# Kernel optimization log

Hardware: AMD Instinct MI355X
Metric: run time of the kernel (lower is better)

## Reference

```python
import jax, jax.numpy as jnp
import numpy as np

D_MODEL = 1024
NUM_HEADS = 16
HEAD_DIM = D_MODEL // NUM_HEADS  # 64
ROPE_THETA = 10000.0
BATCH = 2
SEQ = 2048
NEG_INF = -1e30


def setup_inputs() -> dict:
    key = jax.random.key(0)
    ks = jax.random.split(key, 6)
    std = 1.0 / np.sqrt(D_MODEL)
    x = jax.random.normal(ks[0], (BATCH, SEQ, D_MODEL), dtype=jnp.float32)
    wq = jax.random.normal(ks[1], (D_MODEL, D_MODEL), dtype=jnp.float32) * std
    wk = jax.random.normal(ks[2], (D_MODEL, D_MODEL), dtype=jnp.float32) * std
    wv = jax.random.normal(ks[3], (D_MODEL, D_MODEL), dtype=jnp.float32) * std
    wo = jax.random.normal(ks[4], (D_MODEL, D_MODEL), dtype=jnp.float32) * std
    token_positions = jnp.broadcast_to(jnp.arange(SEQ, dtype=jnp.int32)[None, :], (BATCH, SEQ))
    return {"x": x, "token_positions": token_positions, "wq": wq, "wk": wk, "wv": wv, "wo": wo}


def _apply_rope(t, token_positions):
    # t: (B, H, S, head_dim), token_positions: (B, S)
    half = HEAD_DIM // 2
    inv_freq = 1.0 / (ROPE_THETA ** (2.0 * jnp.arange(half, dtype=jnp.float32) / HEAD_DIM))
    angles = token_positions.astype(jnp.float32)[..., None] * inv_freq  # (B, S, half)
    cos = jnp.cos(angles)[:, None, :, :]  # (B, 1, S, half)
    sin = jnp.sin(angles)[:, None, :, :]
    tp = t.reshape(*t.shape[:-1], half, 2)  # interleaved pairs
    x1, x2 = tp[..., 0], tp[..., 1]
    r1 = x1 * cos - x2 * sin
    r2 = x1 * sin + x2 * cos
    return jnp.stack([r1, r2], axis=-1).reshape(t.shape)


def reference(x, token_positions, wq, wk, wv, wo):
    B, S, D = x.shape
    H, hd = NUM_HEADS, HEAD_DIM
    # projections (Linear: y = x @ W.T, no bias)
    q = (x @ wq.T).reshape(B, S, H, hd).transpose(0, 2, 1, 3)  # (B, H, S, hd)
    k = (x @ wk.T).reshape(B, S, H, hd).transpose(0, 2, 1, 3)
    v = (x @ wv.T).reshape(B, S, H, hd).transpose(0, 2, 1, 3)
    # RoPE on Q, K
    q = _apply_rope(q, token_positions)
    k = _apply_rope(k, token_positions)
    # causal scaled dot-product attention
    scores = jnp.einsum("bhqd,bhkd->bhqk", q, k) / jnp.sqrt(jnp.float32(hd))
    mask = jnp.tril(jnp.ones((S, S), dtype=bool))
    scores = jnp.where(mask, scores, NEG_INF)
    probs = jax.nn.softmax(scores, axis=-1)
    attn = jnp.einsum("bhqk,bhkd->bhqd", probs, v)  # (B, H, S, hd)
    attn = attn.transpose(0, 2, 1, 3).reshape(B, S, D)
    return attn @ wo.T
```

## Files before the change

### kernel.cpp

```cpp
#include <hip/hip_runtime.h>
#include <stdint.h>
#include <math.h>

#define SEQ 2048
#define NH 16
#define DM 1024

typedef __bf16 bf16x8 __attribute__((ext_vector_type(8)));
typedef __bf16 bf16x2 __attribute__((ext_vector_type(2)));
typedef short s16x4 __attribute__((ext_vector_type(4)));
typedef short s16x8 __attribute__((ext_vector_type(8)));
typedef float f32x4 __attribute__((ext_vector_type(4)));
typedef float f32x2 __attribute__((ext_vector_type(2)));

#define ASM_VMCNT0  asm volatile("s_waitcnt vmcnt(0)" ::: "memory")
#define ASM_BARRIER asm volatile("s_barrier" ::: "memory")

__device__ __forceinline__ unsigned short f2bf(float f) {
  union { float f; unsigned u; } v; v.f = f;
  unsigned r = v.u + 0x7fffu + ((v.u >> 16) & 1u);
  return (unsigned short)(r >> 16);
}
__device__ __forceinline__ unsigned pk2(float a, float b) {
  f32x2 v = {a, b};
  bf16x2 r = __builtin_convertvector(v, bf16x2);
  union { bf16x2 h; unsigned u; } c; c.h = r;
  return c.u;
}
__device__ __forceinline__ void load_lds16(const void* g, void* l) {
  __builtin_amdgcn_global_load_lds((__attribute__((address_space(1))) void*)g,
                                   (__attribute__((address_space(3))) void*)l,
                                   16, 0, 0);
}

__global__ void cvt_all(const float* __restrict__ x, const float* __restrict__ wq,
                        const float* __restrict__ wk, const float* __restrict__ wv,
                        const float* __restrict__ wo, unsigned short* __restrict__ ws) {
  const int i = blockIdx.x * blockDim.x + threadIdx.x;
  const int off = i * 4;
  const float* src;
  unsigned short* dst;
  if (off < 4194304) {
    src = x + off;  dst = ws + off;
  } else {
    const int r = off - 4194304;
    const int w = r >> 20, o = r & 1048575;
    const float* tabs[4] = {wq, wk, wv, wo};
    src = tabs[w] + o;  dst = ws + 4194304 + (w << 20) + o;
  }
  const float4 v = *(const float4*)src;
  uint2 u;
  u.x = pk2(v.x, v.y);
  u.y = pk2(v.z, v.w);
  *(uint2*)dst = u;
}

__launch_bounds__(256, 3)
__global__ void gemm_qkv(const unsigned short* __restrict__ X,
                         const unsigned short* __restrict__ W3,
                         unsigned short* __restrict__ Qr,
                         unsigned short* __restrict__ Kr,
                         unsigned short* __restrict__ Vt,
                         const int* __restrict__ tp) {
  __shared__ __align__(16) char smem[32768];

  const int t = threadIdx.x;
  const int lane = t & 63, wave = t >> 6;
  const int quad = lane >> 4, l16 = lane & 15;
  const int m0 = blockIdx.y * 128, n0 = blockIdx.x * 128;
  const int wm = (wave >> 1) * 64, wn = (wave & 1) * 64;

  f32x4 acc[4][4];
#pragma unroll
  for (int i = 0; i < 4; i++)
#pragma unroll
    for (int j = 0; j < 4; j++) { acc[i][j][0]=0.f; acc[i][j][1]=0.f; acc[i][j][2]=0.f; acc[i][j][3]=0.f; }

  const int rr = t >> 2;
  const int cc = (t & 3) * 8;

#define QKV_STAGE(bufidx, k0_) do {                                               \
    char* a_ = smem + (bufidx) * 8192;                                            \
    char* b_ = smem + 16384 + (bufidx) * 8192;                                    \
    _Pragma("unroll")                                                             \
    for (int i_ = 0; i_ < 2; i_++) {                                              \
      load_lds16(X  + (uint64_t)(m0 + i_ * 64 + rr) * 1024 + (k0_) + cc,          \
                 a_ + i_ * 4096 + wave * 1024);                                   \
      load_lds16(W3 + (uint64_t)(n0 + i_ * 64 + rr) * 1024 + (k0_) + cc,          \
                 b_ + i_ * 4096 + wave * 1024);                                   \
    }                                                                             \
  } while (0)

  QKV_STAGE(0, 0);

  for (int k0 = 0; k0 < 1024; k0 += 32) {
    const int buf = (k0 >> 5) & 1;
    ASM_VMCNT0;
    ASM_BARRIER;
    if (k0 + 32 < 1024) QKV_STAGE(buf ^ 1, k0 + 32);
    char* As = smem + buf * 8192;
    char* Bs = smem + 16384 + buf * 8192;

    bf16x8 af[4], bfr[4];
#pragma unroll
    for (int i = 0; i < 4; i++) {
      af[i]  = *(const bf16x8*)(As + (wm + i * 16 + l16) * 64 + quad * 16);
      bfr[i] = *(const bf16x8*)(Bs + (wn + i * 16 + l16) * 64 + quad * 16);
    }
#pragma unroll
    for (int i = 0; i < 4; i++)
#pragma unroll
      for (int j = 0; j < 4; j++)
        acc[i][j] = __builtin_amdgcn_mfma_f32_16x16x32_bf16(af[i], bfr[j], acc[i][j], 0, 0, 0);
  }
#undef QKV_STAGE

  if (n0 < 2048) {
    unsigned short* dst = (n0 < 1024) ? Qr : Kr;
    float fr[4]; int dd[4], hh[4];
#pragma unroll
    for (int j = 0; j < 4; j++) {
      const int n = n0 + wn + j * 16 + l16;
      dd[j] = n & 63;
      hh[j] = (n & 1023) >> 6;
      fr[j] = __builtin_amdgcn_exp2f(-0.20762050594f * (float)(dd[j] & ~1)) * 0.15915494309f;
    }
    const float sgnodd = (l16 & 1) ? 1.f : -1.f;
#pragma unroll
    for (int i = 0; i < 4; i++) {
#pragma unroll
      for (int r = 0; r < 4; r++) {
        const int m = m0 + wm + i * 16 + quad * 4 + r;
        const int s = m & 2047, b = m >> 11;
        const float posf = (float)tp[m];
#pragma unroll
        for (int j = 0; j < 4; j++) {
          const float v = acc[i][j][r];
          const float p = __shfl_xor(v, 1);
          float rev = posf * fr[j];
          rev -= floorf(rev);
          float sn, cs;
          asm("v_sin_f32 %0, %1" : "=v"(sn) : "v"(rev));
          asm("v_cos_f32 %0, %1" : "=v"(cs) : "v"(rev));
          const float rv = fmaf(v, cs, p * sn * sgnodd);
          dst[((uint64_t)((b * NH + hh[j]) * SEQ + s)) * 64 + dd[j]] = f2bf(rv);
        }
      }
    }
  } else {
#pragma unroll
    for (int i = 0; i < 4; i++) {
      const int m = m0 + wm + i * 16 + quad * 4;
      const int s = m & 2047, b = m >> 11;
      const int sl = s & 63;
      const int qv = (sl >> 2) & 3, nv = sl >> 4;
      const int g = (s & ~63) + qv * 16 + (nv >> 1) * 8 + (nv & 1) * 4;
#pragma unroll
      for (int j = 0; j < 4; j++) {
        const int n = n0 - 2048 + wn + j * 16 + l16;
        const int h = n >> 6, d = n & 63;
        uint2 w;
        w.x = pk2(acc[i][j][0], acc[i][j][1]);
        w.y = pk2(acc[i][j][2], acc[i][j][3]);
        *(uint2*)(Vt + ((uint64_t)((b * NH + h) * 64 + d)) * SEQ + g) = w;
      }
    }
  }
}

__launch_bounds__(256, 2)
__global__ void gemm_ao(const unsigned short* __restrict__ A,
                        const unsigned short* __restrict__ B,
                        float* __restrict__ C) {
  __shared__ __align__(16) char smem[32768];

  const int t = threadIdx.x;
  const int lane = t & 63, wave = t >> 6;
  const int quad = lane >> 4, l16 = lane & 15;
  const int m0 = blockIdx.y * 128, n0 = blockIdx.x * 128;
  const int wm = (wave >> 1) * 64, wn = (wave & 1) * 64;

  f32x4 acc[4][4];
#pragma unroll
  for (int i = 0; i < 4; i++)
#pragma unroll
    for (int j = 0; j < 4; j++) { acc[i][j][0]=0.f; acc[i][j][1]=0.f; acc[i][j][2]=0.f; acc[i][j][3]=0.f; }

  const int rr = t >> 2;
  const int cc = (t & 3) * 8;

#define AO_STAGE(bufidx, k0_) do {                                               \
    char* a_ = smem + (bufidx) * 8192;                                            \
    char* b_ = smem + 16384 + (bufidx) * 8192;                                    \
    _Pragma("unroll")                                                             \
    for (int i_ = 0; i_ < 2; i_++) {                                              \
      load_lds16(A + (uint64_t)(m0 + i_ * 64 + rr) * 1024 + (k0_) + cc,           \
                 a_ + i_ * 4096 + wave * 1024);                                   \
      load_lds16(B + (uint64_t)(n0 + i_ * 64 + rr) * 1024 + (k0_) + cc,           \
                 b_ + i_ * 4096 + wave * 1024);                                   \
    }                                                                             \
  } while (0)

  AO_STAGE(0, 0);

  for (int k0 = 0; k0 < 1024; k0 += 32) {
    const int buf = (k0 >> 5) & 1;
    ASM_VMCNT0;
    ASM_BARRIER;
    if (k0 + 32 < 1024) AO_STAGE(buf ^ 1, k0 + 32);
    char* As = smem + buf * 8192;
    char* Bs = smem + 16384 + buf * 8192;

    bf16x8 af[4], bfr[4];
#pragma unroll
    for (int i = 0; i < 4; i++) {
      af[i]  = *(const bf16x8*)(As + (wm + i * 16 + l16) * 64 + quad * 16);
      bfr[i] = *(const bf16x8*)(Bs + (wn + i * 16 + l16) * 64 + quad * 16);
    }
#pragma unroll
    for (int i = 0; i < 4; i++)
#pragma unroll
      for (int j = 0; j < 4; j++)
        acc[i][j] = __builtin_amdgcn_mfma_f32_16x16x32_bf16(af[i], bfr[j], acc[i][j], 0, 0, 0);
  }
#undef AO_STAGE

#pragma unroll
  for (int i = 0; i < 4; i++)
#pragma unroll
    for (int j = 0; j < 4; j++)
#pragma unroll
      for (int r = 0; r < 4; r++) {
        const int m = m0 + wm + i * 16 + quad * 4 + r;
        const int n = n0 + wn + j * 16 + l16;
        C[(uint64_t)m * DM + n] = acc[i][j][r];
      }
}

__launch_bounds__(256, 4)
__global__ void flash_attn(const unsigned short* __restrict__ Q,
                           const unsigned short* __restrict__ K,
                           const unsigned short* __restrict__ Vt,
                           unsigned short* __restrict__ Oa) {
  __shared__ __align__(16) char smem[32768];

  const int t = threadIdx.x;
  const int lane = t & 63, wid = t >> 6;
  const int quad = lane >> 4, l16 = lane & 15;
  const int u = blockIdx.x;
  const int tq = 31 - (u >> 5);
  const int bh = u & 31;
  const uint64_t base = (uint64_t)bh * (SEQ * 64);
  const int qb = tq * 64;
  const int ng = tq + 1;
  const int qg = qb + wid * 16 + l16;
  const int b = bh >> 4, h = bh & 15;

  bf16x8 qf[2];
  {
    const unsigned short* qp = Q + base + (uint64_t)qg * 64 + quad * 8;
    qf[0] = *(const bf16x8*)qp;  qf[1] = *(const bf16x8*)(qp + 32);
  }

  f32x4 o[4];
#pragma unroll
  for (int i = 0; i < 4; i++) { o[i][0]=0.f; o[i][1]=0.f; o[i][2]=0.f; o[i][3]=0.f; }
  float lI = 0.f;

  const int sr8 = lane >> 3;
  const int sc = ((lane & 7) ^ sr8) * 8;
  const int swz = (l16 & 7);

#define STAGE(bufidx, kb_) do {                                                   \
    _Pragma("unroll")                                                             \
    for (int i_ = 0; i_ < 2; i_++) {                                              \
      const int r_ = wid * 16 + i_ * 8 + sr8;                                     \
      load_lds16(K  + base + (uint64_t)((kb_) + r_) * 64 + sc,                    \
                 smem + (bufidx) * 8192 + wid * 2048 + i_ * 1024);                \
      load_lds16(Vt + base + (uint64_t)r_ * SEQ + (kb_) + sc,                     \
                 smem + 16384 + (bufidx) * 8192 + wid * 2048 + i_ * 1024);        \
    }                                                                             \
  } while (0)

  STAGE(0, 0);

  const float c1 = 0.18033688011f;

  for (int it = 0; it < ng; it++) {
    const int kb = it * 64;
    const int buf = it & 1;
    ASM_VMCNT0;
    ASM_BARRIER;
    if (it + 1 < ng) STAGE(buf ^ 1, (it + 1) * 64);
    char* ks = smem + buf * 8192;
    char* vs = smem + 16384 + buf * 8192;

    int nbmax = ((qb + wid * 16 + 15 - kb) >> 4) + 1;
    nbmax = nbmax > 4 ? 4 : (nbmax < 0 ? 0 : nbmax);
    const bool diag = (kb + 63) > (qb + wid * 16);

    f32x4 sf[4];
    float ls = 0.f;
#pragma unroll
    for (int nb = 0; nb < 4; nb++) {
      if (nb < nbmax) {
        f32x4 s; s[0]=0.f; s[1]=0.f; s[2]=0.f; s[3]=0.f;
#pragma unroll
        for (int kk = 0; kk < 2; kk++) {
          bf16x8 kfr = *(const bf16x8*)(ks + (nb * 16 + l16) * 128 + (((kk * 4 + quad) ^ swz) * 16));
          s = __builtin_amdgcn_mfma_f32_16x16x32_bf16(kfr, qf[kk], s, 0, 0, 0);
        }
        if (diag) {
#pragma unroll
          for (int r = 0; r < 4; r++) {
            const int key = kb + nb * 16 + quad * 4 + r;
            const float p = (key <= qg) ? __builtin_amdgcn_exp2f(s[r] * c1) : 0.f;
            sf[nb][r] = p;  ls += p;
          }
        } else {
#pragma unroll
          for (int r = 0; r < 4; r++) {
            const float p = __builtin_amdgcn_exp2f(s[r] * c1);
            sf[nb][r] = p;  ls += p;
          }
        }
      }
    }
    lI += ls;

#pragma unroll
    for (int np = 0; np < 2; np++) {
      if (2 * np < nbmax) {
        union { uint2 u; s16x4 h; } p0;
        p0.u.x = pk2(sf[2 * np][0], sf[2 * np][1]);
        p0.u.y = pk2(sf[2 * np][2], sf[2 * np][3]);
        const bool hi = (2 * np + 1 < nbmax);
        union { uint2 u; s16x4 h; } p1;
        if (hi) {
          p1.u.x = pk2(sf[2 * np + 1][0], sf[2 * np + 1][1]);
          p1.u.y = pk2(sf[2 * np + 1][2], sf[2 * np + 1][3]);
        }
#pragma unroll
        for (int db = 0; db < 4; db++) {
          s16x8 vv = *(const s16x8*)(vs + (db * 16 + l16) * 128 +
                                     (((quad * 2 + np) ^ swz) * 16));
          s16x4 vlo = __builtin_shufflevector(vv, vv, 0, 1, 2, 3);
          o[db] = __builtin_amdgcn_mfma_f32_16x16x16bf16_1k(vlo, p0.h, o[db], 0, 0, 0);
          if (hi) {
            s16x4 vhi = __builtin_shufflevector(vv, vv, 4, 5, 6, 7);
            o[db] = __builtin_amdgcn_mfma_f32_16x16x16bf16_1k(vhi, p1.h, o[db], 0, 0, 0);
          }
        }
      }
    }
  }
#undef STAGE

  float lr = lI;
  lr += __shfl_xor(lr, 16);
  lr += __shfl_xor(lr, 32);
  const float invl = 1.0f / lr;
  unsigned short* orow = Oa + ((uint64_t)(b * SEQ + qg)) * DM + h * 64 + quad * 4;
#pragma unroll
  for (int db = 0; db < 4; db++) {
    uint2 w;
    w.x = pk2(o[db][0] * invl, o[db][1] * invl);
    w.y = pk2(o[db][2] * invl, o[db][3] * invl);
    *(uint2*)(orow + db * 16) = w;
  }
}

extern "C" void kernel_launch(void* const* d_in, const int* in_sizes, int n_in,
                              void* d_out, int out_size, void* d_ws, size_t ws_size,
                              hipStream_t stream) {
  const float* x  = (const float*)d_in[0];
  const int* tp   = (const int*)d_in[1];
  const float* wq = (const float*)d_in[2];
  const float* wk = (const float*)d_in[3];
  const float* wv = (const float*)d_in[4];
  const float* wo = (const float*)d_in[5];
  float* out = (float*)d_out;

  unsigned short* ws = (unsigned short*)d_ws;
  unsigned short* xb  = ws;
  unsigned short* w3b = ws + 4194304;
  unsigned short* wob = ws + 7340032;
  unsigned short* Qr  = ws + 8388608;
  unsigned short* Kr  = ws + 12582912;
  unsigned short* Vt  = ws + 16777216;
  unsigned short* At  = ws + 20971520;

  cvt_all<<<8192, 256, 0, stream>>>(x, wq, wk, wv, wo, ws);
  gemm_qkv<<<dim3(24, 32), 256, 0, stream>>>(xb, w3b, Qr, Kr, Vt, tp);
  flash_attn<<<1024, 256, 0, stream>>>(Qr, Kr, Vt, At);
  gemm_ao<<<dim3(8, 32), 256, 0, stream>>>(At, wob, out);
}
```

Measured before the change: 174.2 us.

## Balance causal flash attention by pairing query tiles and splitting KV with combine

Reworks the causal attention work split so each block handles a balanced share of KV tiles. Segment 0 processes short query tile p fully, then starts the long tile 31-p; segment 1 finishes the remaining KV tiles of that long tile. Partial unnormalized outputs and row sums go to a float scratch buffer and are merged by a new combine kernel. This aims to remove the load imbalance and tail effect of triangular work per block, at the cost of an extra launch and extra global traffic for the partials.

```diff
diff --git a/kernel.cpp b/kernel.cpp
--- a/kernel.cpp
+++ b/kernel.cpp
@@ -241,20 +241,24 @@
 __global__ void flash_attn(const unsigned short* __restrict__ Q,
                            const unsigned short* __restrict__ K,
                            const unsigned short* __restrict__ Vt,
-                           unsigned short* __restrict__ Oa) {
+                           unsigned short* __restrict__ Oa,
+                           float* __restrict__ Pt) {
   __shared__ __align__(16) char smem[32768];
 
   const int t = threadIdx.x;
   const int lane = t & 63, wid = t >> 6;
   const int quad = lane >> 4, l16 = lane & 15;
   const int u = blockIdx.x;
-  const int tq = 31 - (u >> 5);
   const int bh = u & 31;
+  const int p = (u >> 5) & 15;
+  const int seg = u >> 9;
   const uint64_t base = (uint64_t)bh * (SEQ * 64);
-  const int qb = tq * 64;
-  const int ng = tq + 1;
-  const int qg = qb + wid * 16 + l16;
   const int b = bh >> 4, h = bh & 15;
+  const int Tb = (31 - p) * 64;
+
+  const int nTot = seg ? 17 : 16;
+  int qb = seg ? Tb : p * 64;
+  int qg = qb + wid * 16 + l16;
 
   bf16x8 qf[2];
   {
@@ -282,16 +286,33 @@
     }                                                                             \
   } while (0)
 
-  STAGE(0, 0);
+#define KB_OF(i_) (seg ? (15 - p + (i_)) : ((i_) <= p ? (i_) : (i_) - p - 1))
+
+#define FINALIZE(qg_) do {                                                        \
+    float lr = lI;                                                                \
+    lr += __shfl_xor(lr, 16);                                                     \
+    lr += __shfl_xor(lr, 32);                                                     \
+    const float invl = 1.0f / lr;                                                 \
+    unsigned short* orow = Oa + ((uint64_t)(b * SEQ + (qg_))) * DM + h * 64 + quad * 4; \
+    _Pragma("unroll")                                                             \
+    for (int db = 0; db < 4; db++) {                                              \
+      uint2 w;                                                                    \
+      w.x = pk2(o[db][0] * invl, o[db][1] * invl);                                \
+      w.y = pk2(o[db][2] * invl, o[db][3] * invl);                                \
+      *(uint2*)(orow + db * 16) = w;                                              \
+    }                                                                             \
+  } while (0)
+
+  STAGE(0, KB_OF(0) * 64);
 
   const float c1 = 0.18033688011f;
 
-  for (int it = 0; it < ng; it++) {
-    const int kb = it * 64;
+  for (int it = 0; it < nTot; it++) {
+    const int kb = KB_OF(it) * 64;
     const int buf = it & 1;
     ASM_VMCNT0;
     ASM_BARRIER;
-    if (it + 1 < ng) STAGE(buf ^ 1, (it + 1) * 64);
+    if (it + 1 < nTot) STAGE(buf ^ 1, KB_OF(it + 1) * 64);
     char* ks = smem + buf * 8192;
     char* vs = smem + 16384 + buf * 8192;
 
@@ -314,14 +335,14 @@
 #pragma unroll
           for (int r = 0; r < 4; r++) {
             const int key = kb + nb * 16 + quad * 4 + r;
-            const float p = (key <= qg) ? __builtin_amdgcn_exp2f(s[r] * c1) : 0.f;
-            sf[nb][r] = p;  ls += p;
+            const float pe = (key <= qg) ? __builtin_amdgcn_exp2f(s[r] * c1) : 0.f;
+            sf[nb][r] = pe;  ls += pe;
           }
         } else {
 #pragma unroll
           for (int r = 0; r < 4; r++) {
-            const float p = __builtin_amdgcn_exp2f(s[r] * c1);
-            sf[nb][r] = p;  ls += p;
+            const float pe = __builtin_amdgcn_exp2f(s[r] * c1);
+            sf[nb][r] = pe;  ls += pe;
           }
         }
       }
@@ -353,20 +374,66 @@
         }
       }
     }
+
+    if (seg == 0 && it == p) {
+      FINALIZE(qg);
+#pragma unroll
+      for (int i = 0; i < 4; i++) { o[i][0]=0.f; o[i][1]=0.f; o[i][2]=0.f; o[i][3]=0.f; }
+      lI = 0.f;
+      if (p < 15) {
+        qb = Tb;
+        qg = qb + wid * 16 + l16;
+        const unsigned short* qp = Q + base + (uint64_t)qg * 64 + quad * 8;
+        qf[0] = *(const bf16x8*)qp;  qf[1] = *(const bf16x8*)(qp + 32);
+      }
+    }
   }
 #undef STAGE
-
-  float lr = lI;
-  lr += __shfl_xor(lr, 16);
-  lr += __shfl_xor(lr, 32);
-  const float invl = 1.0f / lr;
-  unsigned short* orow = Oa + ((uint64_t)(b * SEQ + qg)) * DM + h * 64 + quad * 4;
-#pragma unroll
-  for (int db = 0; db < 4; db++) {
+#undef KB_OF
+
+  if (seg == 1 && p == 15) {
+    FINALIZE(qg);
+  } else if (seg == 1 || p < 15) {
+    float lr = lI;
+    lr += __shfl_xor(lr, 16);
+    lr += __shfl_xor(lr, 32);
+    float* Pp = Pt + ((uint64_t)((bh * 16 + p) * 2 + seg)) * 4160;
+    const int row = wid * 16 + l16;
+#pragma unroll
+    for (int db = 0; db < 4; db++)
+      *(f32x4*)(Pp + row * 64 + db * 16 + quad * 4) = o[db];
+    if (quad == 0) Pp[4096 + row] = lr;
+  }
+#undef FINALIZE
+}
+
+__global__ void flash_combine(const float* __restrict__ Pt,
+                              unsigned short* __restrict__ Oa) {
+  const int p = blockIdx.x;
+  const int bh = blockIdx.y;
+  const int qb = (31 - p) * 64;
+  const int b = bh >> 4, h = bh & 15;
+  const float* P0 = Pt + ((uint64_t)((bh * 16 + p) * 2 + 0)) * 4160;
+  const float* P1 = P0 + 4160;
+  const int tid = threadIdx.x;
+  const int r = tid >> 2, c0 = (tid & 3) * 16;
+  const float l = P0[4096 + r] + P1[4096 + r];
+  const float inv = 1.0f / l;
+  unsigned short* orow = Oa + ((uint64_t)(b * SEQ + qb + r)) * DM + h * 64 + c0;
+#pragma unroll
+  for (int j = 0; j < 2; j++) {
+    f32x4 a0 = *(const f32x4*)(P0 + r * 64 + c0 + j * 8);
+    f32x4 a1 = *(const f32x4*)(P1 + r * 64 + c0 + j * 8);
+    f32x4 b0 = *(const f32x4*)(P0 + r * 64 + c0 + j * 8 + 4);
+    f32x4 b1 = *(const f32x4*)(P1 + r * 64 + c0 + j * 8 + 4);
     uint2 w;
-    w.x = pk2(o[db][0] * invl, o[db][1] * invl);
-    w.y = pk2(o[db][2] * invl, o[db][3] * invl);
-    *(uint2*)(orow + db * 16) = w;
+    w.x = pk2((a0[0] + a1[0]) * inv, (a0[1] + a1[1]) * inv);
+    w.y = pk2((a0[2] + a1[2]) * inv, (a0[3] + a1[3]) * inv);
+    *(uint2*)(orow + j * 8) = w;
+    uint2 w2;
+    w2.x = pk2((b0[0] + b1[0]) * inv, (b0[1] + b1[1]) * inv);
+    w2.y = pk2((b0[2] + b1[2]) * inv, (b0[3] + b1[3]) * inv);
+    *(uint2*)(orow + j * 8 + 4) = w2;
   }
 }
 
@@ -389,9 +456,11 @@
   unsigned short* Kr  = ws + 12582912;
   unsigned short* Vt  = ws + 16777216;
   unsigned short* At  = ws + 20971520;
+  float* Pt = (float*)(ws + 25165824);
 
   cvt_all<<<8192, 256, 0, stream>>>(x, wq, wk, wv, wo, ws);
   gemm_qkv<<<dim3(24, 32), 256, 0, stream>>>(xb, w3b, Qr, Kr, Vt, tp);
-  flash_attn<<<1024, 256, 0, stream>>>(Qr, Kr, Vt, At);
+  flash_attn<<<1024, 256, 0, stream>>>(Qr, Kr, Vt, At, Pt);
+  flash_combine<<<dim3(15, 32), 256, 0, stream>>>(Pt, At);
   gemm_ao<<<dim3(8, 32), 256, 0, stream>>>(At, wob, out);
 }
```

New measurement: 175.7 us. Within noise of the previous version (+0.8%).
